# Kernel optimization log

Measured on AMD Instinct MI355X. Metric: run time of the kernel, lower is better.

## Reference

```python
import jax, jax.numpy as jnp
import numpy as np

D_MODEL, D_Q, D_K, D_V, N = 1024, 128, 128, 128, 8192

def setup_inputs() -> dict:
    key = jax.random.key(0)
    ks = jax.random.split(key, 7)
    s = 1.0 / np.sqrt(D_MODEL)
    return {
        "x": jax.random.normal(ks[0], (N, D_MODEL), dtype=jnp.float32),
        "Wq": jax.random.uniform(ks[1], (D_MODEL, D_Q), jnp.float32, -s, s),
        "bq": jax.random.uniform(ks[2], (D_Q,), jnp.float32, -s, s),
        "Wk": jax.random.uniform(ks[3], (D_MODEL, D_K), jnp.float32, -s, s),
        "bk": jax.random.uniform(ks[4], (D_K,), jnp.float32, -s, s),
        "Wv": jax.random.uniform(ks[5], (D_MODEL, D_V), jnp.float32, -s, s),
        "bv": jax.random.uniform(ks[6], (D_V,), jnp.float32, -s, s),
    }

def reference(x, Wq, bq, Wk, bk, Wv, bv):
    q = x @ Wq + bq          # [N, d_q]
    k = x @ Wk + bk          # [N, d_k]
    v = x @ Wv + bv          # [N, d_v]
    scale = jnp.sqrt(jnp.asarray(q.shape[-1], q.dtype))
    scores = (q @ k.T) / scale          # [N, N]
    attn = jax.nn.softmax(scores, axis=1)  # matches nn.Softmax(dim=1) on 2D
    return attn @ v                     # [N, d_v]
```

## Files before the change

### kernel.cpp

```cpp
#include <hip/hip_runtime.h>


typedef __attribute__((ext_vector_type(8))) short bf16x8;
typedef __attribute__((ext_vector_type(4))) float f32x4;

#define NTOK 8192
#define DMODEL 1024
#define DH 128
#define NSPLIT 8
#define CPS 16

__device__ __forceinline__ unsigned short f2bf(float f) {
  unsigned int u = __builtin_bit_cast(unsigned int, f);
  u += 0x7fffu + ((u >> 16) & 1u);
  return (unsigned short)(u >> 16);
}

__device__ __forceinline__ unsigned int pack2bf(float a, float b) {
  return (unsigned int)f2bf(a) | ((unsigned int)f2bf(b) << 16);
}

__device__ __forceinline__ void gl2lds16(const void* gp, void* lp) {
  const __attribute__((address_space(1))) unsigned int* g =
      (const __attribute__((address_space(1))) unsigned int*)gp;
  __attribute__((address_space(3))) unsigned int* l =
      (__attribute__((address_space(3))) unsigned int*)lp;
  __builtin_amdgcn_global_load_lds(g, l, 16, 0, 0);
}

__global__ __launch_bounds__(256) void k_build_wt(const float* __restrict__ Wq,
                                                  const float* __restrict__ Wk,
                                                  const float* __restrict__ Wv,
                                                  unsigned short* __restrict__ wt) {
  __shared__ unsigned short tile[32 * 130];
  int k0 = blockIdx.x * 32;
  int p = blockIdx.y;
  int t = threadIdx.x;
  const float* W = (p == 0) ? Wq : ((p == 1) ? Wk : Wv);
  float vscale = (p == 2) ? 0.0625f : 1.0f;
#pragma unroll
  for (int i = 0; i < 16; i++) {
    int e = i * 256 + t;
    int n = e & 127, kk = e >> 7;
    tile[kk * 130 + n] = f2bf(W[(size_t)(k0 + kk) * DH + n] * vscale);
  }
  __syncthreads();
#pragma unroll
  for (int i = 0; i < 16; i++) {
    int e = i * 256 + t;
    int kk = e & 31, n = e >> 5;
    wt[(size_t)(p * DH + n) * DMODEL + k0 + kk] = tile[kk * 130 + n];
  }
}

__global__ __launch_bounds__(256, 2) void k_qkv(const float* __restrict__ x,
                                                const unsigned short* __restrict__ wt,
                                                const float* __restrict__ bq,
                                                const float* __restrict__ bk,
                                                const float* __restrict__ bv,
                                                unsigned short* __restrict__ qs,
                                                unsigned short* __restrict__ kkv,
                                                unsigned short* __restrict__ vt) {
  __shared__ float xt[2][64 * 64];
  __shared__ unsigned short wtt[2][128 * 64];
  int mt = blockIdx.x, p = blockIdx.y;
  int tid = threadIdx.x;
  int w = tid >> 6, lane = tid & 63, l16 = lane & 15, g = lane >> 4;

#define STAGE_QKV(buf, k0)                                                     \
  {                                                                            \
    _Pragma("unroll") for (int r = 0; r < 4; r++) {                            \
      int seg = r * 4 + w;                                                     \
      int xr = seg * 4 + (lane >> 4);                                          \
      int xlc = ((lane & 15) ^ (xr & 15)) & 15;                                \
      gl2lds16(&x[(size_t)(mt * 64 + xr) * DMODEL + (k0) + xlc * 4],           \
               &xt[buf][seg * 256]);                                           \
      int wc = seg * 8 + (lane >> 3);                                          \
      int wlc = ((lane & 7) ^ (wc & 7)) & 7;                                   \
      gl2lds16(&wt[(size_t)(p * DH + wc) * DMODEL + (k0) + wlc * 8],           \
               &wtt[buf][seg * 512]);                                          \
    }                                                                          \
  }

  f32x4 zero = {0.f, 0.f, 0.f, 0.f};
  f32x4 acc[8];
#pragma unroll
  for (int i = 0; i < 8; i++) acc[i] = zero;

  STAGE_QKV(0, 0);
  int arow = w * 16 + l16;
  for (int kt2 = 0; kt2 < 16; kt2++) {
    int b = kt2 & 1;
    __syncthreads();
    if (kt2 < 15) STAGE_QKV(b ^ 1, (kt2 + 1) * 64);

    bf16x8 a[2];
#pragma unroll
    for (int half = 0; half < 2; half++) {
      int lc0 = half * 8 + g * 2;
      const f32x4 u0 = *(const f32x4*)&xt[b][arow * 64 + ((lc0 ^ l16) & 15) * 4];
      const f32x4 u1 = *(const f32x4*)&xt[b][arow * 64 + (((lc0 + 1) ^ l16) & 15) * 4];
      union { unsigned int u[4]; bf16x8 v; } pk;
      pk.u[0] = pack2bf(u0[0], u0[1]);
      pk.u[1] = pack2bf(u0[2], u0[3]);
      pk.u[2] = pack2bf(u1[0], u1[1]);
      pk.u[3] = pack2bf(u1[2], u1[3]);
      a[half] = pk.v;
    }
#pragma unroll
    for (int nt = 0; nt < 8; nt++) {
      int col = nt * 16 + l16;
#pragma unroll
      for (int half = 0; half < 2; half++) {
        int lc = half * 4 + g;
        bf16x8 bf = *(const bf16x8*)&wtt[b][col * 64 + ((lc ^ (col & 7)) & 7) * 8];
        acc[nt] = __builtin_amdgcn_mfma_f32_16x16x32_bf16(a[half], bf, acc[nt], 0, 0, 0);
      }
    }
  }
#undef STAGE_QKV

  const float* bias = (p == 0) ? bq : ((p == 1) ? bk : bv);
  float mult = (p == 0) ? (0.08838834764831845f * 1.44269504088896340f) : 1.0f;
  if (p < 2) {
    unsigned short* outp = (p == 0) ? qs : kkv;
#pragma unroll
    for (int nt = 0; nt < 8; nt++) {
      int col = nt * 16 + l16;
      float bsv = bias[col];
#pragma unroll
      for (int r = 0; r < 4; r++) {
        int row = mt * 64 + w * 16 + g * 4 + r;
        outp[(size_t)row * DH + col] = f2bf((acc[nt][r] + bsv) * mult);
      }
    }
  } else {
#pragma unroll
    for (int nt = 0; nt < 8; nt++) {
      int col = nt * 16 + l16;
      float bsv = bias[col] * 0.0625f;
      int row0 = mt * 64 + w * 16 + g * 4;
      uint2 uv;
      uv.x = pack2bf(acc[nt][0] + bsv, acc[nt][1] + bsv);
      uv.y = pack2bf(acc[nt][2] + bsv, acc[nt][3] + bsv);
      *(uint2*)(&vt[(size_t)col * NTOK + row0]) = uv;
    }
  }
}

__global__ __launch_bounds__(256, 2) void k_flash(const unsigned short* __restrict__ qs,
                                                  const unsigned short* __restrict__ kkv,
                                                  const unsigned short* __restrict__ vt,
                                                  _Float16* __restrict__ opart,
                                                  float* __restrict__ lpart) {
  __shared__ unsigned short kt[2][64 * 128];
  __shared__ unsigned short vtl[2][128 * 64];
  __shared__ unsigned short pscr[4 * 2 * 1024];
  int sp = blockIdx.x, qt = blockIdx.y;
  int tid = threadIdx.x;
  int w = tid >> 6, lane = tid & 63, l16 = lane & 15, g = lane >> 4;
  int swz2 = (l16 & 7) ^ ((l16 >> 3) << 1);

  bf16x8 qf[2][4];
  int qbase = qt * 128 + w * 32;
#pragma unroll
  for (int q2 = 0; q2 < 2; q2++)
#pragma unroll
    for (int f = 0; f < 4; f++)
      qf[q2][f] = *(const bf16x8*)(&qs[(size_t)(qbase + q2 * 16 + l16) * DH + f * 32 + g * 8]);

  int pcK[4], pcV[2], pcP[2];
#pragma unroll
  for (int f = 0; f < 4; f++) {
    int lc = f * 4 + g;
    pcK[f] = (lc & 8) | ((lc ^ l16) & 7);
  }
#pragma unroll
  for (int kb = 0; kb < 2; kb++) {
    int lc = kb * 4 + g;
    pcV[kb] = (lc ^ l16) & 7;
    pcP[kb] = (lc ^ swz2) & 7;
  }

#define STAGE_FLASH(buf, chunk)                                                 \
  {                                                                             \
    int key0 = (chunk) * 64;                                                    \
    _Pragma("unroll") for (int ii = 0; ii < 4; ii++) {                          \
      int i = w * 4 + ii;                                                       \
      int krow = 4 * i + (lane >> 4);                                           \
      int klc = ((lane & 15) & 8) | (((lane & 15) ^ krow) & 7);                 \
      gl2lds16(&kkv[(size_t)(key0 + krow) * DH + klc * 8], &kt[buf][i * 512]);  \
      int vrow = 8 * i + (lane >> 3);                                           \
      int vlc = ((lane & 7) ^ vrow) & 7;                                        \
      gl2lds16(&vt[(size_t)vrow * NTOK + key0 + vlc * 8], &vtl[buf][i * 512]);  \
    }                                                                           \
  }

  f32x4 zero = {0.f, 0.f, 0.f, 0.f};
  f32x4 o[2][8];
#pragma unroll
  for (int q2 = 0; q2 < 2; q2++)
#pragma unroll
    for (int dt = 0; dt < 8; dt++) o[q2][dt] = zero;
  float l[2] = {0.f, 0.f};

  int c0 = sp * CPS;
  STAGE_FLASH(0, c0);

  for (int it = 0; it < CPS; it++) {
    int b = it & 1;
    __syncthreads();
    if (it + 1 < CPS) STAGE_FLASH(b ^ 1, c0 + it + 1);

    f32x4 s[2][4];
#pragma unroll
    for (int q2 = 0; q2 < 2; q2++)
#pragma unroll
      for (int mt = 0; mt < 4; mt++) s[q2][mt] = zero;
#pragma unroll
    for (int mt = 0; mt < 4; mt++) {
      bf16x8 kf[4];
#pragma unroll
      for (int f = 0; f < 4; f++)
        kf[f] = *(const bf16x8*)(&kt[b][(mt * 16 + l16) * 128 + pcK[f] * 8]);
#pragma unroll
      for (int f = 0; f < 4; f++) {
        s[0][mt] = __builtin_amdgcn_mfma_f32_16x16x32_bf16(kf[f], qf[0][f], s[0][mt], 0, 0, 0);
        s[1][mt] = __builtin_amdgcn_mfma_f32_16x16x32_bf16(kf[f], qf[1][f], s[1][mt], 0, 0, 0);
      }
    }

#pragma unroll
    for (int q2 = 0; q2 < 2; q2++) {
      unsigned short* pw = &pscr[(w * 2 + q2) * 1024];
      float ssum = 0.f;
#pragma unroll
      for (int mt = 0; mt < 4; mt++) {
        float p0 = __builtin_amdgcn_exp2f(s[q2][mt][0]);
        float p1 = __builtin_amdgcn_exp2f(s[q2][mt][1]);
        float p2 = __builtin_amdgcn_exp2f(s[q2][mt][2]);
        float p3 = __builtin_amdgcn_exp2f(s[q2][mt][3]);
        ssum += (p0 + p1) + (p2 + p3);
        uint2 uv;
        uv.x = pack2bf(p0, p1);
        uv.y = pack2bf(p2, p3);
        int ch = ((mt * 2 + (g >> 1)) ^ swz2) & 7;
        *(uint2*)(&pw[l16 * 64 + ch * 8 + (g & 1) * 4]) = uv;
      }
      l[q2] += ssum;
    }

    bf16x8 pb[2][2];
#pragma unroll
    for (int q2 = 0; q2 < 2; q2++)
#pragma unroll
      for (int kb = 0; kb < 2; kb++)
        pb[q2][kb] = *(const bf16x8*)(&pscr[(w * 2 + q2) * 1024 + l16 * 64 + pcP[kb] * 8]);

#pragma unroll
    for (int dt = 0; dt < 8; dt++)
#pragma unroll
      for (int kb = 0; kb < 2; kb++) {
        bf16x8 vf = *(const bf16x8*)(&vtl[b][(dt * 16 + l16) * 64 + pcV[kb] * 8]);
        o[0][dt] = __builtin_amdgcn_mfma_f32_16x16x32_bf16(vf, pb[0][kb], o[0][dt], 0, 0, 0);
        o[1][dt] = __builtin_amdgcn_mfma_f32_16x16x32_bf16(vf, pb[1][kb], o[1][dt], 0, 0, 0);
      }
  }
#undef STAGE_FLASH

#pragma unroll
  for (int q2 = 0; q2 < 2; q2++) {
    l[q2] += __shfl_xor(l[q2], 16);
    l[q2] += __shfl_xor(l[q2], 32);
    int qrow = qbase + q2 * 16 + l16;
    size_t obase = ((size_t)sp * NTOK + qrow) * DH;
#pragma unroll
    for (int dt = 0; dt < 8; dt++) {
      union { _Float16 h[4]; uint2 u; } pk;
      pk.h[0] = (_Float16)o[q2][dt][0];
      pk.h[1] = (_Float16)o[q2][dt][1];
      pk.h[2] = (_Float16)o[q2][dt][2];
      pk.h[3] = (_Float16)o[q2][dt][3];
      *(uint2*)(&opart[obase + dt * 16 + g * 4]) = pk.u;
    }
    if (g == 0) lpart[sp * NTOK + qrow] = l[q2];
  }
}

__global__ __launch_bounds__(256) void k_merge(const _Float16* __restrict__ opart,
                                               const float* __restrict__ lpart,
                                               float* __restrict__ out) {
  int gid = blockIdx.x * 256 + threadIdx.x;
  int row = gid >> 6, cp = gid & 63;
  float den = 0.f, n0 = 0.f, n1 = 0.f;
#pragma unroll
  for (int s = 0; s < NSPLIT; s++) {
    den += lpart[s * NTOK + row];
    union { unsigned int u; _Float16 h[2]; } v;
    v.u = *(const unsigned int*)&opart[((size_t)s * NTOK + row) * DH + cp * 2];
    n0 += (float)v.h[0];
    n1 += (float)v.h[1];
  }
  float inv = 16.0f / den;
  *(float2*)&out[(size_t)row * DH + cp * 2] = make_float2(n0 * inv, n1 * inv);
}

extern "C" void kernel_launch(void* const* d_in, const int* in_sizes, int n_in,
                              void* d_out, int out_size, void* d_ws, size_t ws_size,
                              hipStream_t stream) {
  const float* x  = (const float*)d_in[0];
  const float* Wq = (const float*)d_in[1];
  const float* bq = (const float*)d_in[2];
  const float* Wk = (const float*)d_in[3];
  const float* bk = (const float*)d_in[4];
  const float* Wv = (const float*)d_in[5];
  const float* bv = (const float*)d_in[6];
  float* out = (float*)d_out;

  char* ws = (char*)d_ws;
  _Float16*       opart = (_Float16*)(ws);
  unsigned short* wt  = (unsigned short*)(ws + 16777216);
  unsigned short* qsb = (unsigned short*)(ws + 17563648);
  unsigned short* kkb = (unsigned short*)(ws + 19660800);
  unsigned short* vtb = (unsigned short*)(ws + 21757952);
  float* lpart = (float*)(ws + 23855104);

  k_build_wt<<<dim3(32, 3), 256, 0, stream>>>(Wq, Wk, Wv, wt);
  k_qkv<<<dim3(128, 3), 256, 0, stream>>>(x, wt, bq, bk, bv, qsb, kkb, vtb);
  k_flash<<<dim3(NSPLIT, 64), 256, 0, stream>>>(qsb, kkb, vtb, opart, lpart);
  k_merge<<<2048, 256, 0, stream>>>(opart, lpart, out);
}
```

Measured before the change: 150.4 us.

## Shrink QKV projection tiles to 32 rows and add MFMA priority hints in flash

The QKV projection kernel now computes 32-row tiles instead of 64. Each wave owns a 32-column slice of the output and covers both 16-row sub-tiles, the grid goes from 384 to 768 blocks, and the occupancy hint rises to 3 blocks per CU. The grid is also reordered so the three projections for the same rows launch next to each other, which may improve L2 reuse of x. Separately, the flash kernel raises wave priority with s_setprio around its two MFMA phases so matrix work is scheduled ahead of other waves. The risks are that smaller tiles reload the weight tile more often per output, and that the priority hints can starve other waves' memory or softmax phases.

```diff
diff --git a/kernel.cpp b/kernel.cpp
--- a/kernel.cpp
+++ b/kernel.cpp
@@ -53,7 +53,7 @@
   }
 }
 
-__global__ __launch_bounds__(256, 2) void k_qkv(const float* __restrict__ x,
+__global__ __launch_bounds__(256, 3) void k_qkv(const float* __restrict__ x,
                                                 const unsigned short* __restrict__ wt,
                                                 const float* __restrict__ bq,
                                                 const float* __restrict__ bk,
@@ -61,20 +61,23 @@
                                                 unsigned short* __restrict__ qs,
                                                 unsigned short* __restrict__ kkv,
                                                 unsigned short* __restrict__ vt) {
-  __shared__ float xt[2][64 * 64];
+  __shared__ float xt[2][32 * 64];
   __shared__ unsigned short wtt[2][128 * 64];
-  int mt = blockIdx.x, p = blockIdx.y;
+  int p = blockIdx.x, mt0 = blockIdx.y;
   int tid = threadIdx.x;
   int w = tid >> 6, lane = tid & 63, l16 = lane & 15, g = lane >> 4;
 
 #define STAGE_QKV(buf, k0)                                                     \
   {                                                                            \
-    _Pragma("unroll") for (int r = 0; r < 4; r++) {                            \
+    _Pragma("unroll") for (int r = 0; r < 2; r++) {                            \
       int seg = r * 4 + w;                                                     \
       int xr = seg * 4 + (lane >> 4);                                          \
       int xlc = ((lane & 15) ^ (xr & 15)) & 15;                                \
-      gl2lds16(&x[(size_t)(mt * 64 + xr) * DMODEL + (k0) + xlc * 4],           \
+      gl2lds16(&x[(size_t)(mt0 * 32 + xr) * DMODEL + (k0) + xlc * 4],          \
                &xt[buf][seg * 256]);                                           \
+    }                                                                          \
+    _Pragma("unroll") for (int r = 0; r < 4; r++) {                            \
+      int seg = r * 4 + w;                                                     \
       int wc = seg * 8 + (lane >> 3);                                          \
       int wlc = ((lane & 7) ^ (wc & 7)) & 7;                                   \
       gl2lds16(&wt[(size_t)(p * DH + wc) * DMODEL + (k0) + wlc * 8],           \
@@ -83,38 +86,44 @@
   }
 
   f32x4 zero = {0.f, 0.f, 0.f, 0.f};
-  f32x4 acc[8];
-#pragma unroll
-  for (int i = 0; i < 8; i++) acc[i] = zero;
+  f32x4 acc[2][2];
+#pragma unroll
+  for (int i = 0; i < 2; i++)
+#pragma unroll
+    for (int j = 0; j < 2; j++) acc[i][j] = zero;
 
   STAGE_QKV(0, 0);
-  int arow = w * 16 + l16;
   for (int kt2 = 0; kt2 < 16; kt2++) {
     int b = kt2 & 1;
     __syncthreads();
     if (kt2 < 15) STAGE_QKV(b ^ 1, (kt2 + 1) * 64);
 
-    bf16x8 a[2];
-#pragma unroll
-    for (int half = 0; half < 2; half++) {
-      int lc0 = half * 8 + g * 2;
-      const f32x4 u0 = *(const f32x4*)&xt[b][arow * 64 + ((lc0 ^ l16) & 15) * 4];
-      const f32x4 u1 = *(const f32x4*)&xt[b][arow * 64 + (((lc0 + 1) ^ l16) & 15) * 4];
-      union { unsigned int u[4]; bf16x8 v; } pk;
-      pk.u[0] = pack2bf(u0[0], u0[1]);
-      pk.u[1] = pack2bf(u0[2], u0[3]);
-      pk.u[2] = pack2bf(u1[0], u1[1]);
-      pk.u[3] = pack2bf(u1[2], u1[3]);
-      a[half] = pk.v;
-    }
-#pragma unroll
-    for (int nt = 0; nt < 8; nt++) {
-      int col = nt * 16 + l16;
+    bf16x8 a[2][2];
+#pragma unroll
+    for (int mt = 0; mt < 2; mt++) {
+      int arow = mt * 16 + l16;
+#pragma unroll
+      for (int half = 0; half < 2; half++) {
+        int lc0 = half * 8 + g * 2;
+        const f32x4 u0 = *(const f32x4*)&xt[b][arow * 64 + ((lc0 ^ l16) & 15) * 4];
+        const f32x4 u1 = *(const f32x4*)&xt[b][arow * 64 + (((lc0 + 1) ^ l16) & 15) * 4];
+        union { unsigned int u[4]; bf16x8 v; } pk;
+        pk.u[0] = pack2bf(u0[0], u0[1]);
+        pk.u[1] = pack2bf(u0[2], u0[3]);
+        pk.u[2] = pack2bf(u1[0], u1[1]);
+        pk.u[3] = pack2bf(u1[2], u1[3]);
+        a[mt][half] = pk.v;
+      }
+    }
+#pragma unroll
+    for (int nt = 0; nt < 2; nt++) {
+      int col = (w * 2 + nt) * 16 + l16;
 #pragma unroll
       for (int half = 0; half < 2; half++) {
         int lc = half * 4 + g;
         bf16x8 bf = *(const bf16x8*)&wtt[b][col * 64 + ((lc ^ (col & 7)) & 7) * 8];
-        acc[nt] = __builtin_amdgcn_mfma_f32_16x16x32_bf16(a[half], bf, acc[nt], 0, 0, 0);
+        acc[0][nt] = __builtin_amdgcn_mfma_f32_16x16x32_bf16(a[0][half], bf, acc[0][nt], 0, 0, 0);
+        acc[1][nt] = __builtin_amdgcn_mfma_f32_16x16x32_bf16(a[1][half], bf, acc[1][nt], 0, 0, 0);
       }
     }
   }
@@ -125,25 +134,30 @@
   if (p < 2) {
     unsigned short* outp = (p == 0) ? qs : kkv;
 #pragma unroll
-    for (int nt = 0; nt < 8; nt++) {
-      int col = nt * 16 + l16;
+    for (int nt = 0; nt < 2; nt++) {
+      int col = (w * 2 + nt) * 16 + l16;
       float bsv = bias[col];
 #pragma unroll
-      for (int r = 0; r < 4; r++) {
-        int row = mt * 64 + w * 16 + g * 4 + r;
-        outp[(size_t)row * DH + col] = f2bf((acc[nt][r] + bsv) * mult);
-      }
+      for (int mt = 0; mt < 2; mt++)
+#pragma unroll
+        for (int r = 0; r < 4; r++) {
+          int row = mt0 * 32 + mt * 16 + g * 4 + r;
+          outp[(size_t)row * DH + col] = f2bf((acc[mt][nt][r] + bsv) * mult);
+        }
     }
   } else {
 #pragma unroll
-    for (int nt = 0; nt < 8; nt++) {
-      int col = nt * 16 + l16;
+    for (int nt = 0; nt < 2; nt++) {
+      int col = (w * 2 + nt) * 16 + l16;
       float bsv = bias[col] * 0.0625f;
-      int row0 = mt * 64 + w * 16 + g * 4;
-      uint2 uv;
-      uv.x = pack2bf(acc[nt][0] + bsv, acc[nt][1] + bsv);
-      uv.y = pack2bf(acc[nt][2] + bsv, acc[nt][3] + bsv);
-      *(uint2*)(&vt[(size_t)col * NTOK + row0]) = uv;
+#pragma unroll
+      for (int mt = 0; mt < 2; mt++) {
+        int row0 = mt0 * 32 + mt * 16 + g * 4;
+        uint2 uv;
+        uv.x = pack2bf(acc[mt][nt][0] + bsv, acc[mt][nt][1] + bsv);
+        uv.y = pack2bf(acc[mt][nt][2] + bsv, acc[mt][nt][3] + bsv);
+        *(uint2*)(&vt[(size_t)col * NTOK + row0]) = uv;
+      }
     }
   }
 }
@@ -217,6 +231,7 @@
     for (int q2 = 0; q2 < 2; q2++)
 #pragma unroll
       for (int mt = 0; mt < 4; mt++) s[q2][mt] = zero;
+    __builtin_amdgcn_s_setprio(1);
 #pragma unroll
     for (int mt = 0; mt < 4; mt++) {
       bf16x8 kf[4];
@@ -229,6 +244,7 @@
         s[1][mt] = __builtin_amdgcn_mfma_f32_16x16x32_bf16(kf[f], qf[1][f], s[1][mt], 0, 0, 0);
       }
     }
+    __builtin_amdgcn_s_setprio(0);
 
 #pragma unroll
     for (int q2 = 0; q2 < 2; q2++) {
@@ -257,6 +273,7 @@
       for (int kb = 0; kb < 2; kb++)
         pb[q2][kb] = *(const bf16x8*)(&pscr[(w * 2 + q2) * 1024 + l16 * 64 + pcP[kb] * 8]);
 
+    __builtin_amdgcn_s_setprio(1);
 #pragma unroll
     for (int dt = 0; dt < 8; dt++)
 #pragma unroll
@@ -265,6 +282,7 @@
         o[0][dt] = __builtin_amdgcn_mfma_f32_16x16x32_bf16(vf, pb[0][kb], o[0][dt], 0, 0, 0);
         o[1][dt] = __builtin_amdgcn_mfma_f32_16x16x32_bf16(vf, pb[1][kb], o[1][dt], 0, 0, 0);
       }
+    __builtin_amdgcn_s_setprio(0);
   }
 #undef STAGE_FLASH
 
@@ -326,7 +344,7 @@
   float* lpart = (float*)(ws + 23855104);
 
   k_build_wt<<<dim3(32, 3), 256, 0, stream>>>(Wq, Wk, Wv, wt);
-  k_qkv<<<dim3(128, 3), 256, 0, stream>>>(x, wt, bq, bk, bv, qsb, kkb, vtb);
+  k_qkv<<<dim3(3, 256), 256, 0, stream>>>(x, wt, bq, bk, bv, qsb, kkb, vtb);
   k_flash<<<dim3(NSPLIT, 64), 256, 0, stream>>>(qsb, kkb, vtb, opart, lpart);
   k_merge<<<2048, 256, 0, stream>>>(opart, lpart, out);
 }
```

After: 155.1 us. 1.03x slower.
